# Kernel optimization log

Hardware: AMD Instinct MI355X
Metric: run time of the kernel (lower is better)

The kernel has to match this reference:

```python
import jax, jax.numpy as jnp
import numpy as np

B, C, S, L = 8, 512, 2048, 8921


def setup_inputs() -> dict:
    key = jax.random.key(0)
    k1, k2, k3, k4, k5 = jax.random.split(key, 5)
    return {
        "encoded": jax.random.normal(k1, (B, C, S), dtype=jnp.float32),
        "W_attn": jax.random.normal(k2, (L, C), dtype=jnp.float32) * 0.02,
        "b_attn": jax.random.normal(k3, (L,), dtype=jnp.float32) * 0.02,
        "W_cls": jax.random.normal(k4, (L, C), dtype=jnp.float32) * 0.02,
        "b_cls": jax.random.normal(k5, (L,), dtype=jnp.float32) * 0.02,
    }


def reference(encoded, W_attn, b_attn, W_cls, b_cls):
    # encoded: (B, C, S). Linear over channels after transpose -> scores (B, S, L)
    scores = jnp.einsum("bcs,lc->bsl", encoded, W_attn) + b_attn
    # softmax over the sequence dimension (dim=1 of (B, S, L))
    weights = jax.nn.softmax(scores, axis=1)
    # context: (B, L, S) @ (B, S, C) -> (B, L, C)
    context = jnp.einsum("bsl,bcs->blc", weights, encoded)
    # per-label diagonal classifier: elementwise multiply with (L, C) weight, reduce C
    logits = jnp.sum(context * W_cls, axis=2) + b_cls  # (B, L)
    return logits
```

## Files before the change

kernel.cpp:

```cpp
#include <hip/hip_runtime.h>
#include <hip/hip_bf16.h>
#include <stdint.h>

#define B_ 8
#define C_ 512
#define S_ 2048
#define L_ 8921
#define LTILE 128
#define NLT 70
#define NSC 16
#define ROUNDS 16

using f32x16 = __attribute__((ext_vector_type(16))) float;
using s16x8  = __attribute__((ext_vector_type(8))) short;

static __device__ __forceinline__ unsigned short f2bf(float f) {
    union { float f; uint32_t u; } a; a.f = f;
    uint32_t u = a.u;
    return (unsigned short)((u + 0x7fffu + ((u >> 16) & 1u)) >> 16);
}

__global__ void cvt_w(const float* __restrict__ src, unsigned short* __restrict__ dst, int n4) {
    int i = blockIdx.x * 256 + threadIdx.x;
    if (i >= n4) return;
    float4 v = ((const float4*)src)[i];
    ushort4 o;
    o.x = f2bf(v.x); o.y = f2bf(v.y); o.z = f2bf(v.z); o.w = f2bf(v.w);
    ((ushort4*)dst)[i] = o;
}

__global__ void cvt_e(const float* __restrict__ enc, unsigned short* __restrict__ ebt) {
    __shared__ float tile[64][65];
    int x = blockIdx.x;
    int ct = (x & 7) * 64;
    int st = ((x >> 3) & 31) * 64;
    int b  = x >> 8;
    int t = threadIdx.x;
    const float* src = enc + (size_t)b * C_ * S_;
    #pragma unroll
    for (int it = 0; it < 16; ++it) {
        int idx = it * 256 + t;
        int rc = idx >> 6, rs = idx & 63;
        tile[rc][rs] = src[(size_t)(ct + rc) * S_ + st + rs];
    }
    __syncthreads();
    unsigned short* dst = ebt + (size_t)b * S_ * C_;
    #pragma unroll
    for (int it = 0; it < 16; ++it) {
        int idx = it * 256 + t;
        int rs = idx >> 6, rc = idx & 63;
        dst[(size_t)(st + rs) * C_ + ct + rc] = f2bf(tile[rc][rs]);
    }
}

__global__ __launch_bounds__(256, 2) void attn_main(
    const unsigned short* __restrict__ ebt,
    const unsigned short* __restrict__ wa,
    const unsigned short* __restrict__ wc,
    float* __restrict__ pnum, float* __restrict__ pden)
{
    __shared__ __align__(16) unsigned char sE[16384];

    const int tid  = threadIdx.x;
    const int lane = tid & 63;
    const int wave = tid >> 6;

    const int x   = blockIdx.x;
    const int i8  = x & 7;
    const int t9  = x >> 3;
    const int jj9 = t9 % 9;
    const int bsc = t9 / 9;
    const int lt  = jj9 * 8 + i8;
    const int b   = bsc & 7;
    const int sc  = bsc >> 3;
    const int l0  = lt * LTILE;
    const int s0  = sc * 128;

    const int h = lane >> 5;
    int glRow = l0 + wave * 32 + (lane & 31);
    if (glRow > L_ - 1) glRow = L_ - 1;
    const unsigned short* waRow = wa + (size_t)glRow * C_ + h * 8;
    const unsigned short* wcRow = wc + (size_t)glRow * C_ + h * 8;

    const int slRow  = lane >> 2;
    const int srcCk  = (((lane & 3) ^ ((slRow >> 1) & 3)) << 3);
    const unsigned short* eg0 = ebt + ((size_t)b * S_ + s0 + (wave * 2) * 16 + slRow) * C_ + srcCk;
    const unsigned short* eg1 = eg0 + (size_t)16 * C_;
    const int ldst0 = (wave * 2) * 1024 + slRow * 64 + (lane & 3) * 16;
    const int ldst1 = ldst0 + 1024;

    auto stage = [&](int rr) {
        const int c0 = rr * 32;
        const int bufo = (rr & 1) << 13;
        __builtin_amdgcn_global_load_lds(
            (__attribute__((address_space(1))) void*)(eg0 + c0),
            (__attribute__((address_space(3))) void*)(sE + bufo + ldst0), 16, 0, 0);
        __builtin_amdgcn_global_load_lds(
            (__attribute__((address_space(1))) void*)(eg1 + c0),
            (__attribute__((address_space(3))) void*)(sE + bufo + ldst1), 16, 0, 0);
    };

    struct WREG { s16x8 a0, a1, c0, c1; };
    auto loadW = [&](int rr) -> WREG {
        const int co = rr * 32;
        WREG w;
        w.a0 = *(const s16x8*)(waRow + co);
        w.a1 = *(const s16x8*)(waRow + co + 16);
        w.c0 = *(const s16x8*)(wcRow + co);
        w.c1 = *(const s16x8*)(wcRow + co + 16);
        return w;
    };

    const int rowB  = (lane & 31) * 64;
    const int swz   = (lane >> 1) & 3;

    f32x16 accS[4], accV[4];
    #pragma unroll
    for (int nf = 0; nf < 4; ++nf)
        #pragma unroll
        for (int r = 0; r < 16; ++r) { accS[nf][r] = 0.f; accV[nf][r] = 0.f; }

    stage(0);
    WREG wcur = loadW(0);

    for (int rr = 0; rr < ROUNDS; ++rr) {
        __syncthreads();
        if (rr + 1 < ROUNDS) stage(rr + 1);
        WREG wnxt = (rr + 1 < ROUNDS) ? loadW(rr + 1) : wcur;

        const unsigned char* db = sE + ((rr & 1) << 13);
        {
            s16x8 fe[4];
            #pragma unroll
            for (int nf = 0; nf < 4; ++nf) {
                const int off = (nf << 11) + rowB + (((0 + h) ^ swz) << 4);
                fe[nf] = *(const s16x8*)(db + off);
            }
            #pragma unroll
            for (int nf = 0; nf < 4; ++nf) {
                accS[nf] = __builtin_amdgcn_mfma_f32_32x32x16_bf16(wcur.a0, fe[nf], accS[nf], 0, 0, 0);
                accV[nf] = __builtin_amdgcn_mfma_f32_32x32x16_bf16(wcur.c0, fe[nf], accV[nf], 0, 0, 0);
            }
        }
        {
            s16x8 fe[4];
            #pragma unroll
            for (int nf = 0; nf < 4; ++nf) {
                const int off = (nf << 11) + rowB + (((2 + h) ^ swz) << 4);
                fe[nf] = *(const s16x8*)(db + off);
            }
            #pragma unroll
            for (int nf = 0; nf < 4; ++nf) {
                accS[nf] = __builtin_amdgcn_mfma_f32_32x32x16_bf16(wcur.a1, fe[nf], accS[nf], 0, 0, 0);
                accV[nf] = __builtin_amdgcn_mfma_f32_32x32x16_bf16(wcur.c1, fe[nf], accV[nf], 0, 0, 0);
            }
        }
        wcur = wnxt;
    }

    float numA[16], denA[16];
    #pragma unroll
    for (int r = 0; r < 16; ++r) { numA[r] = 0.f; denA[r] = 0.f; }
    #pragma unroll
    for (int nf = 0; nf < 4; ++nf)
        #pragma unroll
        for (int r = 0; r < 16; ++r) {
            float e = __expf(accS[nf][r]);
            denA[r] += e;
            numA[r] += e * accV[nf][r];
        }
    if (lt < NLT) {
        const size_t obase = ((size_t)((b * NLT + lt) * NSC + sc)) * LTILE;
        #pragma unroll
        for (int r = 0; r < 16; ++r) {
            float n = numA[r], d = denA[r];
            n += __shfl_xor(n, 1);   d += __shfl_xor(d, 1);
            n += __shfl_xor(n, 2);   d += __shfl_xor(d, 2);
            n += __shfl_xor(n, 4);   d += __shfl_xor(d, 4);
            n += __shfl_xor(n, 8);   d += __shfl_xor(d, 8);
            n += __shfl_xor(n, 16);  d += __shfl_xor(d, 16);
            if ((lane & 31) == 0) {
                int row = wave * 32 + (r & 3) + 8 * (r >> 2) + 4 * h;
                pnum[obase + row] = n;
                pden[obase + row] = d;
            }
        }
    }
}

__global__ void finalize(const float* __restrict__ pnum, const float* __restrict__ pden,
                         const float* __restrict__ bcls, float* __restrict__ out) {
    int gid = blockIdx.x * 256 + threadIdx.x;
    if (gid >= B_ * L_) return;
    int b = gid / L_, l = gid - b * L_;
    int lt = l >> 7, row = l & 127;
    float n = 0.f, d = 0.f;
    #pragma unroll
    for (int s = 0; s < NSC; ++s) {
        size_t idx = ((size_t)((b * NLT + lt) * NSC + s)) * LTILE + row;
        n += pnum[idx];
        d += pden[idx];
    }
    out[gid] = n / d + bcls[l];
}

extern "C" void kernel_launch(void* const* d_in, const int* in_sizes, int n_in,
                              void* d_out, int out_size, void* d_ws, size_t ws_size,
                              hipStream_t stream) {
    (void)in_sizes; (void)n_in; (void)out_size; (void)ws_size;
    const float* enc  = (const float*)d_in[0];
    const float* Wa   = (const float*)d_in[1];
    const float* Wc   = (const float*)d_in[3];
    const float* bcls = (const float*)d_in[4];

    unsigned char* ws = (unsigned char*)d_ws;
    const size_t oEbt = 0;
    const size_t oWa  = oEbt + 16777216;
    const size_t oWc  = oWa + 9136128;
    const size_t oPn  = oWc + 9136128;
    const size_t oPd  = oPn + 4587520;

    unsigned short* ebt  = (unsigned short*)(ws + oEbt);
    unsigned short* waBf = (unsigned short*)(ws + oWa);
    unsigned short* wcBf = (unsigned short*)(ws + oWc);
    float* pnum = (float*)(ws + oPn);
    float* pden = (float*)(ws + oPd);

    const int n4 = (L_ * C_) / 4;
    cvt_w<<<(n4 + 255) / 256, 256, 0, stream>>>(Wa, waBf, n4);
    cvt_w<<<(n4 + 255) / 256, 256, 0, stream>>>(Wc, wcBf, n4);
    cvt_e<<<B_ * 32 * 8, 256, 0, stream>>>(enc, ebt);
    attn_main<<<128 * 9 * 8, 256, 0, stream>>>(ebt, waBf, wcBf, pnum, pden);
    finalize<<<(B_ * L_ + 255) / 256, 256, 0, stream>>>(pnum, pden, bcls, (float*)d_out);
}
```

Baseline: 474.0 us.

## Load encoded tiles directly from global into registers, dropping LDS staging

The attention GEMM kernel stops staging encoded rows through LDS with global_load_lds and barriers. Each wave now loads its own encoded fragments straight from global memory into registers, double-buffered over a fully unrolled loop. This removes the LDS traffic and __syncthreads, but the four waves of a block each load the same encoded data, so global and L2 traffic goes up. Register pressure also rises and could hurt occupancy under launch_bounds(256,2).

```diff
diff --git a/kernel.cpp b/kernel.cpp
--- a/kernel.cpp
+++ b/kernel.cpp
@@ -59,8 +59,6 @@
     const unsigned short* __restrict__ wc,
     float* __restrict__ pnum, float* __restrict__ pden)
 {
-    __shared__ __align__(16) unsigned char sE[16384];
-
     const int tid  = threadIdx.x;
     const int lane = tid & 63;
     const int wave = tid >> 6;
@@ -81,81 +79,52 @@
     if (glRow > L_ - 1) glRow = L_ - 1;
     const unsigned short* waRow = wa + (size_t)glRow * C_ + h * 8;
     const unsigned short* wcRow = wc + (size_t)glRow * C_ + h * 8;
-
-    const int slRow  = lane >> 2;
-    const int srcCk  = (((lane & 3) ^ ((slRow >> 1) & 3)) << 3);
-    const unsigned short* eg0 = ebt + ((size_t)b * S_ + s0 + (wave * 2) * 16 + slRow) * C_ + srcCk;
-    const unsigned short* eg1 = eg0 + (size_t)16 * C_;
-    const int ldst0 = (wave * 2) * 1024 + slRow * 64 + (lane & 3) * 16;
-    const int ldst1 = ldst0 + 1024;
-
-    auto stage = [&](int rr) {
-        const int c0 = rr * 32;
-        const int bufo = (rr & 1) << 13;
-        __builtin_amdgcn_global_load_lds(
-            (__attribute__((address_space(1))) void*)(eg0 + c0),
-            (__attribute__((address_space(3))) void*)(sE + bufo + ldst0), 16, 0, 0);
-        __builtin_amdgcn_global_load_lds(
-            (__attribute__((address_space(1))) void*)(eg1 + c0),
-            (__attribute__((address_space(3))) void*)(sE + bufo + ldst1), 16, 0, 0);
+    const unsigned short* eRow[4];
+    #pragma unroll
+    for (int nf = 0; nf < 4; ++nf)
+        eRow[nf] = ebt + ((size_t)b * S_ + s0 + nf * 32 + (lane & 31)) * C_ + h * 8;
+
+    auto loadRound = [&](int rr, s16x8* wv, s16x8 (*ev)[2]) {
+        const int co = rr * 32;
+        wv[0] = *(const s16x8*)(waRow + co);
+        wv[1] = *(const s16x8*)(waRow + co + 16);
+        wv[2] = *(const s16x8*)(wcRow + co);
+        wv[3] = *(const s16x8*)(wcRow + co + 16);
+        #pragma unroll
+        for (int nf = 0; nf < 4; ++nf) {
+            ev[nf][0] = *(const s16x8*)(eRow[nf] + co);
+            ev[nf][1] = *(const s16x8*)(eRow[nf] + co + 16);
+        }
     };
 
-    struct WREG { s16x8 a0, a1, c0, c1; };
-    auto loadW = [&](int rr) -> WREG {
-        const int co = rr * 32;
-        WREG w;
-        w.a0 = *(const s16x8*)(waRow + co);
-        w.a1 = *(const s16x8*)(waRow + co + 16);
-        w.c0 = *(const s16x8*)(wcRow + co);
-        w.c1 = *(const s16x8*)(wcRow + co + 16);
-        return w;
+    f32x16 accS[4], accV[4];
+    #pragma unroll
+    for (int nf = 0; nf < 4; ++nf)
+        #pragma unroll
+        for (int r = 0; r < 16; ++r) { accS[nf][r] = 0.f; accV[nf][r] = 0.f; }
+
+    auto mfmaRound = [&](const s16x8* wv, const s16x8 (*ev)[2]) {
+        #pragma unroll
+        for (int nf = 0; nf < 4; ++nf) {
+            accS[nf] = __builtin_amdgcn_mfma_f32_32x32x16_bf16(wv[0], ev[nf][0], accS[nf], 0, 0, 0);
+            accV[nf] = __builtin_amdgcn_mfma_f32_32x32x16_bf16(wv[2], ev[nf][0], accV[nf], 0, 0, 0);
+        }
+        #pragma unroll
+        for (int nf = 0; nf < 4; ++nf) {
+            accS[nf] = __builtin_amdgcn_mfma_f32_32x32x16_bf16(wv[1], ev[nf][1], accS[nf], 0, 0, 0);
+            accV[nf] = __builtin_amdgcn_mfma_f32_32x32x16_bf16(wv[3], ev[nf][1], accV[nf], 0, 0, 0);
+        }
     };
 
-    const int rowB  = (lane & 31) * 64;
-    const int swz   = (lane >> 1) & 3;
-
-    f32x16 accS[4], accV[4];
-    #pragma unroll
-    for (int nf = 0; nf < 4; ++nf)
-        #pragma unroll
-        for (int r = 0; r < 16; ++r) { accS[nf][r] = 0.f; accV[nf][r] = 0.f; }
-
-    stage(0);
-    WREG wcur = loadW(0);
-
-    for (int rr = 0; rr < ROUNDS; ++rr) {
-        __syncthreads();
-        if (rr + 1 < ROUNDS) stage(rr + 1);
-        WREG wnxt = (rr + 1 < ROUNDS) ? loadW(rr + 1) : wcur;
-
-        const unsigned char* db = sE + ((rr & 1) << 13);
-        {
-            s16x8 fe[4];
-            #pragma unroll
-            for (int nf = 0; nf < 4; ++nf) {
-                const int off = (nf << 11) + rowB + (((0 + h) ^ swz) << 4);
-                fe[nf] = *(const s16x8*)(db + off);
-            }
-            #pragma unroll
-            for (int nf = 0; nf < 4; ++nf) {
-                accS[nf] = __builtin_amdgcn_mfma_f32_32x32x16_bf16(wcur.a0, fe[nf], accS[nf], 0, 0, 0);
-                accV[nf] = __builtin_amdgcn_mfma_f32_32x32x16_bf16(wcur.c0, fe[nf], accV[nf], 0, 0, 0);
-            }
-        }
-        {
-            s16x8 fe[4];
-            #pragma unroll
-            for (int nf = 0; nf < 4; ++nf) {
-                const int off = (nf << 11) + rowB + (((2 + h) ^ swz) << 4);
-                fe[nf] = *(const s16x8*)(db + off);
-            }
-            #pragma unroll
-            for (int nf = 0; nf < 4; ++nf) {
-                accS[nf] = __builtin_amdgcn_mfma_f32_32x32x16_bf16(wcur.a1, fe[nf], accS[nf], 0, 0, 0);
-                accV[nf] = __builtin_amdgcn_mfma_f32_32x32x16_bf16(wcur.c1, fe[nf], accV[nf], 0, 0, 0);
-            }
-        }
-        wcur = wnxt;
+    s16x8 wv0[4], wv1[4];
+    s16x8 ev0[4][2], ev1[4][2];
+    loadRound(0, wv0, ev0);
+    #pragma unroll
+    for (int rr2 = 0; rr2 < ROUNDS / 2; ++rr2) {
+        loadRound(2 * rr2 + 1, wv1, ev1);
+        mfmaRound(wv0, ev0);
+        if (rr2 + 1 < ROUNDS / 2) loadRound(2 * rr2 + 2, wv0, ev0);
+        mfmaRound(wv1, ev1);
     }
 
     float numA[16], denA[16];
```

New measurement: 908.0 us. 91.6% more time.
